# Optimization experiments

Hardware: AMD Instinct MI355X
Metric: run time of the kernel (lower is better)

Reference implementation:

```python
import jax, jax.numpy as jnp
import numpy as np

B, S, D = 32, 512, 1024
DROPNUM = 128


def setup_inputs() -> dict:
    key = jax.random.key(0)
    k1, k2, k3, k4 = jax.random.split(key, 4)
    return {
        "in_seq": jax.random.normal(k1, (B, S, D), dtype=jnp.float32),
        "out_seq": jax.random.normal(k2, (B, S, D), dtype=jnp.float32),
        "drop_idx": jax.random.randint(k3, (B, DROPNUM), 0, S, dtype=jnp.int64),
        "keep_idx": jax.random.randint(k4, (B, S - DROPNUM), 0, S, dtype=jnp.int64),
    }


def reference(in_seq, out_seq, drop_idx, keep_idx):
    b, s, d = in_seq.shape
    dropnum = drop_idx.shape[1]

    # Batched gathers (replaces the per-batch index_select loop)
    predictions = jnp.take_along_axis(out_seq, drop_idx[:, :, None], axis=1)      # (B, dropnum, D)
    inputs = jnp.take_along_axis(in_seq, keep_idx[:, :, None], axis=1)            # (B, S-dropnum, D)
    reconstructions = jnp.take_along_axis(out_seq, keep_idx[:, :, None], axis=1)  # (B, S-dropnum, D)

    # target[i, j] = i*S + drop_idx[i, j]
    target = (jnp.arange(b, dtype=drop_idx.dtype)[:, None] * s + drop_idx).reshape(-1)  # (B*dropnum,)

    outputs = predictions.reshape(b * dropnum, d)
    keys = in_seq.reshape(b * s, d)
    # torch: outputs @ in_seq.permute(2,0,1).reshape(D, B*S)  ==  outputs @ keys.T
    lossmat = jnp.einsum("nd,md->nm", outputs, keys)  # (B*dropnum, B*S)

    # Accuracy (no-grad diagnostic in original)
    top1 = jnp.argmax(lossmat, axis=1)
    acc = jnp.mean((top1 == target).astype(jnp.float32)) * 100.0

    # Cross entropy (mean reduction, as nn.CrossEntropyLoss default)
    logp = jax.nn.log_softmax(lossmat, axis=1)
    xe = -jnp.mean(logp[jnp.arange(b * dropnum), target])

    # MSE (mean reduction)
    mse = jnp.mean((inputs - reconstructions) ** 2)

    loss = xe + mse
    return (loss, xe, mse, acc)
```

## Files before the change

kernel.cpp:

```cpp
#include <hip/hip_runtime.h>
#include <hip/hip_bf16.h>


typedef __attribute__((ext_vector_type(8))) _Float16 half8;
typedef __attribute__((ext_vector_type(4))) _Float16 half4v;
typedef __attribute__((ext_vector_type(4))) float f32x4;

#define MFMA16(a, b, c) __builtin_amdgcn_mfma_f32_16x16x32_f16((a), (b), (c), 0, 0, 0)

__device__ __forceinline__ float fexp2(float x) {
    float r;
    asm("v_exp_f32 %0, %1" : "=v"(r) : "v"(x));
    return r;
}
__device__ __forceinline__ float flog2(float x) {
    float r;
    asm("v_log_f32 %0, %1" : "=v"(r) : "v"(x));
    return r;
}

__device__ __forceinline__ void glds16(const _Float16* g, _Float16* l) {
    __builtin_amdgcn_global_load_lds(
        (const __attribute__((address_space(1))) unsigned int*)g,
        (__attribute__((address_space(3))) unsigned int*)l, 16, 0, 0);
}

__global__ void conv_k(const float* __restrict__ in_seq, const float* __restrict__ out_seq,
                       const int* __restrict__ drop, _Float16* __restrict__ Kf,
                       _Float16* __restrict__ Pf, int* __restrict__ tgt) {
    const float C = 1.4426950408889634f;
    unsigned bid = blockIdx.x;
    if (bid < 16384u) {
        unsigned t = bid * 256u + threadIdx.x;
        unsigned idx = t * 4u;
        unsigned row = idx >> 10;
        unsigned k = idx & 1023u;
        float4 v = *(const float4*)(in_seq + idx);
        unsigned d = (row << 10) + (k ^ (((row >> 1) & 3u) << 3));
        half4v o = {(_Float16)v.x, (_Float16)v.y, (_Float16)v.z, (_Float16)v.w};
        *(half4v*)(Kf + d) = o;
    } else {
        unsigned t = (bid - 16384u) * 256u + threadIdx.x;
        unsigned idx = t * 4u;
        unsigned prow = idx >> 10;
        unsigned k = idx & 1023u;
        unsigned b = prow >> 7, j = prow & 127u;
        int srow = drop[b * 128u + j];
        size_t gsrc = ((size_t)((b << 9) + (unsigned)srow) << 10) + k;
        float4 v = *(const float4*)(out_seq + gsrc);
        unsigned d = (prow << 10) + (k ^ (((prow >> 1) & 3u) << 3));
        half4v o = {(_Float16)(v.x * C), (_Float16)(v.y * C), (_Float16)(v.z * C),
                    (_Float16)(v.w * C)};
        *(half4v*)(Pf + d) = o;
        if (k == 0) tgt[prow] = (int)((b << 9) + (unsigned)srow);
    }
}

__global__ __launch_bounds__(512, 2) void gemm_stats_k(
    const _Float16* __restrict__ Pf, const _Float16* __restrict__ Kf,
    const int* __restrict__ tgt,
    float* __restrict__ pmax, float* __restrict__ psum, int* __restrict__ pidx,
    float* __restrict__ xt) {
    extern __shared__ _Float16 lds[];

    const int tid = threadIdx.x;
    const int lane = tid & 63;
    const int wave = tid >> 6;
    const int wm = wave >> 2, wn = wave & 3;
    const int lr = lane & 15, lk = lane >> 4;

    unsigned id = blockIdx.x;
    unsigned wg = (id & 7u) * 128u + (id >> 3);
    const int bn = wg >> 4, bm = wg & 15;

    const _Float16* aSrc = Pf + (size_t)(bm * 256 + (tid >> 2)) * 1024 + (tid & 3) * 8;
    const _Float16* bSrc = Kf + (size_t)(bn * 256 + (tid >> 2)) * 1024 + (tid & 3) * 8;

    const unsigned swz = (unsigned)((lk ^ ((lr >> 1) & 3)) << 3);

    f32x4 acc[8][4] = {};
    half8 bfr[4];

    auto STAGEP = [&](int h, int ph) {
        const int skt = h >> 1, sks = h & 1;
        const unsigned ss = (unsigned)(h & 3) * 16384u;
        const unsigned go = (unsigned)(skt * 64 + sks * 32);
        if (ph == 0) {
            glds16(aSrc + go, &lds[ss + tid * 8]);
            glds16(aSrc + 131072 + go, &lds[ss + 4096 + tid * 8]);
        } else {
            glds16(bSrc + go, &lds[ss + 8192 + tid * 8]);
            glds16(bSrc + 131072 + go, &lds[ss + 12288 + tid * 8]);
        }
    };

    #pragma unroll
    for (int h = 0; h < 4; ++h) {
        STAGEP(h, 0);
        STAGEP(h, 1);
    }
    asm volatile("s_waitcnt vmcnt(12)" ::: "memory");
    __builtin_amdgcn_s_barrier();
    __builtin_amdgcn_sched_barrier(0);

    #pragma unroll
    for (int p = 0; p < 64; ++p) {
        const int q = p & 3;
        const int ks = q >> 1, mh = q & 1;
        const int kt = p >> 2;
        const unsigned sb = (unsigned)((2 * kt + ks) & 3) * 16384u;

        half8 a[4];
        #pragma unroll
        for (int i = 0; i < 4; ++i) {
            int r = wm * 128 + mh * 64 + i * 16 + lr;
            a[i] = *(const half8*)&lds[sb + r * 32 + swz];
        }
        if (q == 0 || q == 2) {
            #pragma unroll
            for (int n = 0; n < 4; ++n) {
                int r = wn * 64 + n * 16 + lr;
                bfr[n] = *(const half8*)&lds[sb + 8192 + r * 32 + swz];
            }
        }
        if (p >= 2 && p <= 57) STAGEP(4 + (p - 2) / 2, (p - 2) & 1);

        __builtin_amdgcn_s_barrier();
        asm volatile("s_waitcnt lgkmcnt(0)" ::: "memory");
        __builtin_amdgcn_sched_barrier(0);

        __builtin_amdgcn_s_setprio(1);
        #pragma unroll
        for (int i = 0; i < 4; ++i)
            #pragma unroll
            for (int n = 0; n < 4; ++n)
                acc[mh * 4 + i][n] = MFMA16(a[i], bfr[n], acc[mh * 4 + i][n]);
        __builtin_amdgcn_s_setprio(0);

        if (p & 1) {
            if (p < 59) {
                asm volatile("s_waitcnt vmcnt(8)" ::: "memory");
            } else if (p == 59) {
                asm volatile("s_waitcnt vmcnt(4)" ::: "memory");
            } else if (p == 61) {
                asm volatile("s_waitcnt vmcnt(0)" ::: "memory");
            }
        }
        if (p < 63) {
            __builtin_amdgcn_s_barrier();
            __builtin_amdgcn_sched_barrier(0);
        }
    }

    const int chunk = bn * 4 + wn;
    #pragma unroll
    for (int mi = 0; mi < 8; ++mi) {
        #pragma unroll
        for (int j = 0; j < 4; ++j) {
            int grow = bm * 256 + wm * 128 + mi * 16 + lk * 4 + j;
            int tcol = tgt[grow];
            float v0 = acc[mi][0][j], v1 = acc[mi][1][j], v2 = acc[mi][2][j],
                  v3 = acc[mi][3][j];
            int c0 = bn * 256 + wn * 64 + lr;
            if (c0 == tcol) xt[grow] = v0;
            if (c0 + 16 == tcol) xt[grow] = v1;
            if (c0 + 32 == tcol) xt[grow] = v2;
            if (c0 + 48 == tcol) xt[grow] = v3;
            float mx = fmaxf(fmaxf(v0, v1), fmaxf(v2, v3));
            #pragma unroll
            for (int off = 1; off < 16; off <<= 1) mx = fmaxf(mx, __shfl_xor(mx, off));
            int am = v0 == mx ? c0
                   : v1 == mx ? c0 + 16
                   : v2 == mx ? c0 + 32
                   : v3 == mx ? c0 + 48
                              : 0x7fffffff;
            #pragma unroll
            for (int off = 1; off < 16; off <<= 1) {
                int o = __shfl_xor(am, off);
                am = o < am ? o : am;
            }
            float s = fexp2(v0 - mx) + fexp2(v1 - mx) + fexp2(v2 - mx) + fexp2(v3 - mx);
            #pragma unroll
            for (int off = 1; off < 16; off <<= 1) s += __shfl_xor(s, off);
            if (lr == 0) {
                pmax[grow * 256 + chunk] = mx;
                psum[grow * 256 + chunk] = s;
                pidx[grow * 256 + chunk] = am;
            }
        }
    }
}

__global__ void pass2_k(const float* __restrict__ pmax, const float* __restrict__ psum,
                        const int* __restrict__ pidx, const float* __restrict__ xt,
                        const int* __restrict__ tgt, float* __restrict__ rxe,
                        float* __restrict__ rhit) {
    int row = blockIdx.x;
    int t = threadIdx.x;
    float m = -3.0e38f, l = 0.f;
    int ai = 0x7fffffff;
    for (int c = t; c < 256; c += 64) {
        float cm = pmax[row * 256 + c];
        float cl = psum[row * 256 + c];
        int ci = pidx[row * 256 + c];
        if (cm > m || (cm == m && ci < ai)) {
            l = l * fexp2(m - cm) + cl;
            ai = ci;
            m = cm;
        } else {
            l += cl * fexp2(cm - m);
        }
    }
    #pragma unroll
    for (int off = 1; off < 64; off <<= 1) {
        float om = __shfl_xor(m, off);
        float ol = __shfl_xor(l, off);
        int oi = __shfl_xor(ai, off);
        if (om > m || (om == m && oi < ai)) {
            l = l * fexp2(m - om) + ol;
            ai = oi;
            m = om;
        } else {
            l += ol * fexp2(om - m);
        }
    }
    if (t == 0) {
        rxe[row] = (m + flog2(l) - xt[row]) * 0.69314718055994531f;
        rhit[row] = (ai == tgt[row]) ? 1.f : 0.f;
    }
}

__global__ void mse_partial_k(const float* __restrict__ inseq, const float* __restrict__ outseq,
                              const int* __restrict__ keep, float* __restrict__ msep) {
    float s = 0.f;
    for (unsigned f = blockIdx.x * 256u + threadIdx.x; f < 3145728u; f += 1024u * 256u) {
        unsigned rowid = f >> 8;
        unsigned kf = (f & 255u) << 2;
        unsigned b = rowid / 384u;
        unsigned j = rowid - b * 384u;
        int r = keep[b * 384u + j];
        size_t base = (((size_t)(b * 512u + (unsigned)r)) << 10) + kf;
        float4 a = *(const float4*)(inseq + base);
        float4 c = *(const float4*)(outseq + base);
        float dx = a.x - c.x, dy = a.y - c.y, dz = a.z - c.z, dw = a.w - c.w;
        s += dx * dx + dy * dy + dz * dz + dw * dw;
    }
    #pragma unroll
    for (int off = 1; off < 64; off <<= 1) s += __shfl_xor(s, off);
    __shared__ float red[4];
    if ((threadIdx.x & 63) == 0) red[threadIdx.x >> 6] = s;
    __syncthreads();
    if (threadIdx.x == 0) msep[blockIdx.x] = red[0] + red[1] + red[2] + red[3];
}

__global__ void finalize_k(const float* __restrict__ rxe, const float* __restrict__ rhit,
                           const float* __restrict__ msep, float* __restrict__ out) {
    int tid = threadIdx.x;
    float sx = 0.f, sh = 0.f, sm = 0.f;
    for (int i = tid; i < 4096; i += 256) {
        sx += rxe[i];
        sh += rhit[i];
    }
    for (int i = tid; i < 1024; i += 256) sm += msep[i];
    #pragma unroll
    for (int off = 1; off < 64; off <<= 1) {
        sx += __shfl_xor(sx, off);
        sh += __shfl_xor(sh, off);
        sm += __shfl_xor(sm, off);
    }
    __shared__ float red[3][4];
    int w = tid >> 6;
    if ((tid & 63) == 0) {
        red[0][w] = sx;
        red[1][w] = sh;
        red[2][w] = sm;
    }
    __syncthreads();
    if (tid == 0) {
        sx = red[0][0] + red[0][1] + red[0][2] + red[0][3];
        sh = red[1][0] + red[1][1] + red[1][2] + red[1][3];
        sm = red[2][0] + red[2][1] + red[2][2] + red[2][3];
        float xe = sx * (1.f / 4096.f);
        float mse = sm / (12288.f * 1024.f);
        float accp = 100.f * sh * (1.f / 4096.f);
        out[0] = xe + mse;
        out[1] = xe;
        out[2] = mse;
        out[3] = accp;
    }
}

extern "C" void kernel_launch(void* const* d_in, const int* in_sizes, int n_in,
                              void* d_out, int out_size, void* d_ws, size_t ws_size,
                              hipStream_t stream) {
    const float* in_seq = (const float*)d_in[0];
    const float* out_seq = (const float*)d_in[1];
    const int* drop = (const int*)d_in[2];
    const int* keep = (const int*)d_in[3];
    float* out = (float*)d_out;

    char* w = (char*)d_ws;
    _Float16* Kf = (_Float16*)w; w += 33554432;
    _Float16* Pf = (_Float16*)w; w += 8388608;
    float* pmax = (float*)w; w += 4194304;
    float* psum = (float*)w; w += 4194304;
    int* pidx = (int*)w; w += 4194304;
    float* xt = (float*)w; w += 16384;
    int* tgt = (int*)w; w += 16384;
    float* rxe = (float*)w; w += 16384;
    float* rhit = (float*)w; w += 16384;
    float* msep = (float*)w; w += 4096;

    static int attr_done = 0;
    if (!attr_done) {
        (void)hipFuncSetAttribute((const void*)gemm_stats_k,
                                  hipFuncAttributeMaxDynamicSharedMemorySize, 131072);
        attr_done = 1;
    }

    conv_k<<<20480, 256, 0, stream>>>(in_seq, out_seq, drop, Kf, Pf, tgt);
    gemm_stats_k<<<1024, 512, 131072, stream>>>(Pf, Kf, tgt, pmax, psum, pidx, xt);
    pass2_k<<<4096, 64, 0, stream>>>(pmax, psum, pidx, xt, tgt, rxe, rhit);
    mse_partial_k<<<1024, 256, 0, stream>>>(in_seq, out_seq, keep, msep);
    finalize_k<<<1, 256, 0, stream>>>(rxe, rhit, msep, out);
}
```

Before: 354.6 us.

## Double-buffer LDS fragment reads to overlap with MFMA across phases

Adds register double buffering for the A and B fragments: the next phase's LDS reads are issued before the current phase's MFMAs, and the per-phase barrier plus lgkmcnt(0) wait before compute is removed. The vmcnt wait points shift to even phases so global-to-LDS staging still completes before those slots are read. The aim is to hide LDS read latency behind matrix math. In exchange it uses more VGPRs, which could lower occupancy, and it depends on the reordered waits and barriers being correct, since LDS reads now run while other waves' staging writes may still be in flight.

```diff
diff --git a/kernel.cpp b/kernel.cpp
--- a/kernel.cpp
+++ b/kernel.cpp
@@ -79,7 +79,7 @@
     const unsigned swz = (unsigned)((lk ^ ((lr >> 1) & 3)) << 3);
 
     f32x4 acc[8][4] = {};
-    half8 bfr[4];
+    half8 abuf[2][4], bbuf[2][4];
 
     auto STAGEP = [&](int h, int ph) {
         const int skt = h >> 1, sks = h & 1;
@@ -94,6 +94,24 @@
         }
     };
 
+    auto LOADA = [&](half8* dst, int p1) {
+        const int mh = p1 & 1;
+        const unsigned sb = (unsigned)((p1 >> 1) & 3) * 16384u;
+        #pragma unroll
+        for (int i = 0; i < 4; ++i) {
+            int r = wm * 128 + mh * 64 + i * 16 + lr;
+            dst[i] = *(const half8*)&lds[sb + r * 32 + swz];
+        }
+    };
+    auto LOADB = [&](half8* dst, int p1) {
+        const unsigned sb = (unsigned)((p1 >> 1) & 3) * 16384u;
+        #pragma unroll
+        for (int n = 0; n < 4; ++n) {
+            int r = wn * 64 + n * 16 + lr;
+            dst[n] = *(const half8*)&lds[sb + 8192 + r * 32 + swz];
+        }
+    };
+
     #pragma unroll
     for (int h = 0; h < 4; ++h) {
         STAGEP(h, 0);
@@ -102,31 +120,14 @@
     asm volatile("s_waitcnt vmcnt(12)" ::: "memory");
     __builtin_amdgcn_s_barrier();
     __builtin_amdgcn_sched_barrier(0);
+    LOADA(abuf[0], 0);
+    LOADB(bbuf[0], 0);
 
     #pragma unroll
     for (int p = 0; p < 64; ++p) {
-        const int q = p & 3;
-        const int ks = q >> 1, mh = q & 1;
-        const int kt = p >> 2;
-        const unsigned sb = (unsigned)((2 * kt + ks) & 3) * 16384u;
-
-        half8 a[4];
-        #pragma unroll
-        for (int i = 0; i < 4; ++i) {
-            int r = wm * 128 + mh * 64 + i * 16 + lr;
-            a[i] = *(const half8*)&lds[sb + r * 32 + swz];
-        }
-        if (q == 0 || q == 2) {
-            #pragma unroll
-            for (int n = 0; n < 4; ++n) {
-                int r = wn * 64 + n * 16 + lr;
-                bfr[n] = *(const half8*)&lds[sb + 8192 + r * 32 + swz];
-            }
-        }
         if (p >= 2 && p <= 57) STAGEP(4 + (p - 2) / 2, (p - 2) & 1);
-
-        __builtin_amdgcn_s_barrier();
-        asm volatile("s_waitcnt lgkmcnt(0)" ::: "memory");
+        if (p < 63) LOADA(abuf[(p + 1) & 1], p + 1);
+        if ((p & 1) && p < 63) LOADB(bbuf[((p + 1) >> 1) & 1], p + 1);
         __builtin_amdgcn_sched_barrier(0);
 
         __builtin_amdgcn_s_setprio(1);
@@ -134,15 +135,18 @@
         for (int i = 0; i < 4; ++i)
             #pragma unroll
             for (int n = 0; n < 4; ++n)
-                acc[mh * 4 + i][n] = MFMA16(a[i], bfr[n], acc[mh * 4 + i][n]);
+                acc[(p & 1) * 4 + i][n] = MFMA16(abuf[p & 1][i], bbuf[(p >> 1) & 1][n],
+                                                 acc[(p & 1) * 4 + i][n]);
         __builtin_amdgcn_s_setprio(0);
 
-        if (p & 1) {
-            if (p < 59) {
+        if (!(p & 1)) {
+            if (p == 0) {
                 asm volatile("s_waitcnt vmcnt(8)" ::: "memory");
-            } else if (p == 59) {
+            } else if (p <= 56) {
+                asm volatile("s_waitcnt vmcnt(6)" ::: "memory");
+            } else if (p == 58) {
                 asm volatile("s_waitcnt vmcnt(4)" ::: "memory");
-            } else if (p == 61) {
+            } else if (p == 60) {
                 asm volatile("s_waitcnt vmcnt(0)" ::: "memory");
             }
         }
```

Result: no change. 352.1 us (-0.7%).
